# Optimization experiments

Measured on AMD Instinct MI355X. Metric: run time of the kernel, lower is better.

## Reference

```python
import jax, jax.numpy as jnp
import numpy as np

N = 100000
IN_C = 256
OUT_C = 128
E = 3200000
NNZ = 3200000
K = 3  # n_wavelets
ATT_H = 64


def spmm(idx, vals, m):
    # idx: [2, nnz] (row, col), vals: [nnz], m: [N, d] -> [N, d]
    rows, cols = idx[0], idx[1]
    return jax.ops.segment_sum(vals[:, None] * m[cols], rows, num_segments=N)


def appnp_k1_a0(h, edge_index):
    # PyG APPNP(K=1, alpha=0) == one gcn-normalized propagation with self-loops
    loops = jnp.arange(N, dtype=edge_index.dtype)
    row = jnp.concatenate([edge_index[0], loops])
    col = jnp.concatenate([edge_index[1], loops])
    ones = jnp.ones(row.shape[0], dtype=h.dtype)
    deg = jax.ops.segment_sum(ones, col, num_segments=N)
    dinv = jnp.where(deg > 0, 1.0 / jnp.sqrt(deg), 0.0)
    norm = dinv[row] * dinv[col]
    return jax.ops.segment_sum(norm[:, None] * h[col], row, num_segments=N)


def setup_inputs() -> dict:
    key = jax.random.key(0)
    ks = jax.random.split(key, 12)
    x = jax.random.normal(ks[0], (N, IN_C), dtype=jnp.float32)
    edge_index = jax.random.randint(ks[1], (2, E), 0, N)
    phi_idx = jax.random.randint(ks[2], (K, 2, NNZ), 0, N)
    phi_vals = jax.random.uniform(ks[3], (K, NNZ), dtype=jnp.float32) * (1.0 / 32.0)
    phi_inv_idx = jax.random.randint(ks[4], (K, 2, NNZ), 0, N)
    phi_inv_vals = jax.random.uniform(ks[5], (K, NNZ), dtype=jnp.float32) * (1.0 / 32.0)
    # learned parameters
    lin_w = jax.random.normal(ks[6], (IN_C, OUT_C), dtype=jnp.float32) * (1.0 / np.sqrt(IN_C))
    lin_b = jnp.zeros((OUT_C,), dtype=jnp.float32)
    gw_w = jax.random.normal(ks[7], (IN_C, OUT_C), dtype=jnp.float32) * (1.0 / np.sqrt(IN_C))
    diag_w = jax.random.uniform(ks[8], (N,), dtype=jnp.float32, minval=0.9, maxval=1.1)
    att_w1 = jax.random.normal(ks[9], (OUT_C, ATT_H), dtype=jnp.float32) * (1.0 / np.sqrt(OUT_C))
    att_b1 = jnp.zeros((ATT_H,), dtype=jnp.float32)
    att_w2 = jax.random.normal(ks[10], (ATT_H, 1), dtype=jnp.float32) * (1.0 / np.sqrt(ATT_H))
    return {"x": x, "edge_index": edge_index, "phi_idx": phi_idx, "phi_vals": phi_vals,
            "phi_inv_idx": phi_inv_idx, "phi_inv_vals": phi_inv_vals,
            "lin_w": lin_w, "lin_b": lin_b, "gw_w": gw_w, "diag_w": diag_w,
            "att_w1": att_w1, "att_b1": att_b1, "att_w2": att_w2}


def reference(x, edge_index, phi_idx, phi_vals, phi_inv_idx, phi_inv_vals,
              lin_w, lin_b, gw_w, diag_w, att_w1, att_b1, att_w2):
    # --- mean branch: Linear -> L2 normalize * 1.8 -> APPNP(K=1, alpha=0)
    mean = x @ lin_w + lin_b
    nrm = jnp.linalg.norm(mean, axis=1, keepdims=True)
    mean = mean / jnp.maximum(nrm, 1e-12) * 1.8
    mean = appnp_k1_a0(mean, edge_index)

    # --- logstd branch: GraphWaveletLayer (activation = identity)
    x_ = x @ gw_w  # [N, OUT_C]
    outs = []
    for i in range(K):
        t = spmm(phi_inv_idx[i], phi_inv_vals[i], x_)
        t = diag_w[:, None] * t
        t = spmm(phi_idx[i], phi_vals[i], t)
        outs.append(t)
    z = jnp.stack(outs, axis=1)  # [N, K, OUT_C]

    # --- attention pooling over wavelet axis
    w = jax.nn.relu(jnp.einsum('nkd,dh->nkh', z, att_w1) + att_b1) @ att_w2  # [N, K, 1]
    beta = jax.nn.softmax(w, axis=1)
    logstd = (beta * z).sum(axis=1)  # [N, OUT_C]
    return (mean, logstd)
```

## Files before the change

### kernel.cpp

```cpp
#include <hip/hip_runtime.h>
#include <hip/hip_bf16.h>
#include <hip/hip_fp16.h>


#define WS_HIST  2
#define WS_BUILD 6
#define WS_GATH  8

__global__ __launch_bounds__(256) void hist_kernel(const int* __restrict__ idx,
                                                   int* __restrict__ cnt, int n) {
    int i = blockIdx.x * 256 + threadIdx.x;
    if (i < n) atomicAdd(&cnt[__builtin_nontemporal_load(idx + i)], 1);
}

__global__ __launch_bounds__(256) void dinv_kernel(int* __restrict__ cnt,
                                                   float* __restrict__ dinv, int n) {
    int i = blockIdx.x * 256 + threadIdx.x;
    if (i < n) { dinv[i] = rsqrtf((float)(cnt[i] + 1)); cnt[i] = 0; }
}

__global__ __launch_bounds__(256) void scan_reduce_kernel(
    const int* __restrict__ cnt, int* __restrict__ bsum, int N) {
    __shared__ int wsum[4];
    int base = blockIdx.x * 1024;
    int t = threadIdx.x;
    int s = 0;
#pragma unroll
    for (int j = 0; j < 4; ++j) {
        int idx = base + t * 4 + j;
        if (idx < N) s += cnt[idx];
    }
#pragma unroll
    for (int off = 32; off; off >>= 1) s += __shfl_xor(s, off);
    int lane = t & 63, w = t >> 6;
    if (lane == 0) wsum[w] = s;
    __syncthreads();
    if (t == 0) bsum[blockIdx.x] = wsum[0] + wsum[1] + wsum[2] + wsum[3];
}

__global__ void scan_bsum_kernel(const int* __restrict__ bsum,
                                 int* __restrict__ bofs,
                                 int* __restrict__ ptr, int nblk, int N) {
    if (threadIdx.x == 0 && blockIdx.x == 0) {
        int run = 0;
        for (int i = 0; i < nblk; ++i) { bofs[i] = run; run += bsum[i]; }
        bofs[nblk] = run;
        ptr[N] = run;
    }
}

__global__ __launch_bounds__(256) void scan_block_kernel(
    int* __restrict__ cnt, const int* __restrict__ bofs,
    int* __restrict__ ptr, int* __restrict__ cursor, int N) {
    __shared__ int wsum[4];
    int base = blockIdx.x * 1024;
    int t = threadIdx.x, lane = t & 63, w = t >> 6;
    int v[4]; int s = 0;
#pragma unroll
    for (int j = 0; j < 4; ++j) {
        int idx = base + t * 4 + j;
        v[j] = (idx < N) ? cnt[idx] : 0;
        s += v[j];
    }
    int incl = s;
#pragma unroll
    for (int off = 1; off < 64; off <<= 1) {
        int nn = __shfl_up(incl, off);
        if (lane >= off) incl += nn;
    }
    if (lane == 63) wsum[w] = incl;
    __syncthreads();
    int wofs = 0;
    for (int i = 0; i < w; ++i) wofs += wsum[i];
    int run = bofs[blockIdx.x] + wofs + incl - s;
#pragma unroll
    for (int j = 0; j < 4; ++j) {
        int idx = base + t * 4 + j;
        if (idx < N) { ptr[idx] = run; cursor[idx] = run; cnt[idx] = 0; }
        run += v[j];
    }
}

__global__ __launch_bounds__(256) void fused_pipe_kernel(
    const int* __restrict__ ptr_g, const int2* __restrict__ cpair_g,
    const __half* __restrict__ src, const float* __restrict__ init_src,
    const float* __restrict__ dinv,
    float* __restrict__ dstf, __half* __restrict__ dsth, int N, int nnz_g,
    const int* __restrict__ rows_b, const int* __restrict__ cols_b,
    const float* __restrict__ vals_b, const float* __restrict__ diag,
    int* __restrict__ cursor_b, unsigned long long* __restrict__ cpair_b,
    int nnz_b, int mode,
    const int* __restrict__ rows_h, int* __restrict__ cnt, int nnz_h,
    int mix)
{
    int role, lid, nloc;
    if (!mix) { role = 2; lid = blockIdx.x; nloc = gridDim.x; }
    else {
        int r = blockIdx.x & 15, g = blockIdx.x >> 4, ng = gridDim.x >> 4;
        if (r < WS_HIST)                { role = 0; lid = g * WS_HIST + r;                nloc = ng * WS_HIST; }
        else if (r < WS_HIST + WS_BUILD){ role = 1; lid = g * WS_BUILD + (r - WS_HIST);   nloc = ng * WS_BUILD; }
        else                            { role = 2; lid = g * WS_GATH + (r - WS_HIST - WS_BUILD); nloc = ng * WS_GATH; }
    }

    if (role == 0) {
        if (!rows_h) return;
        int stride = nloc * 256;
        for (int i = lid * 256 + threadIdx.x; i < nnz_h; i += stride)
            atomicAdd(&cnt[__builtin_nontemporal_load(rows_h + i)], 1);
        return;
    }
    if (role == 1) {
        if (!rows_b) return;
        int stride = nloc * 256;
        for (int i = lid * 256 + threadIdx.x; i < nnz_b; i += stride) {
            int r = __builtin_nontemporal_load(rows_b + i);
            int c = __builtin_nontemporal_load(cols_b + i);
            float v;
            if (mode == 2) v = dinv[r] * dinv[c];
            else {
                v = __builtin_nontemporal_load(vals_b + i);
                if (mode == 1) v *= diag[c];
            }
            int pos = atomicAdd(&cursor_b[r], 1);
            unsigned long long pk =
                ((unsigned long long)(unsigned)__float_as_uint(v) << 32) | (unsigned)c;
            __builtin_nontemporal_store(pk, cpair_b + pos);
        }
        return;
    }

    const int lane = threadIdx.x & 63;
    const size_t lofs = (size_t)(lane * 2);
    int wid = (lid * 256 + threadIdx.x) >> 6;
    const int nwaves = (nloc * 256) >> 6;
    for (int row = wid; row < N; row += nwaves) {
        int s = ptr_g[row], e = ptr_g[row + 1];
        e = min(e, nnz_g); s = max(0, min(s, e));
        float accx = 0.f, accy = 0.f;
        if (init_src) {
            float d = dinv[row];
            float dd = d * d;
            float2 m = *(const float2*)(init_src + (size_t)row * 128 + lofs);
            accx = dd * m.x; accy = dd * m.y;
        }
        for (int base = s; base < e; base += 64) {
            int n = min(64, e - base);
            int2 p = make_int2(0, 0);
            if (lane < n) p = cpair_g[base + lane];
            int j = 0;
            for (; j + 16 <= n; j += 16) {
                __half2 sv[16];
                float vj[16];
#pragma unroll
                for (int u = 0; u < 16; ++u) {
                    int cj = __builtin_amdgcn_readlane(p.x, j + u);
                    vj[u] = __int_as_float(__builtin_amdgcn_readlane(p.y, j + u));
                    sv[u] = *(const __half2*)(src + (size_t)cj * 128 + lofs);
                }
#pragma unroll
                for (int u = 0; u < 16; ++u) {
                    accx += vj[u] * __low2float(sv[u]);
                    accy += vj[u] * __high2float(sv[u]);
                }
            }
            for (; j + 4 <= n; j += 4) {
                __half2 sv[4];
                float vj[4];
#pragma unroll
                for (int u = 0; u < 4; ++u) {
                    int cj = __builtin_amdgcn_readlane(p.x, j + u);
                    vj[u] = __int_as_float(__builtin_amdgcn_readlane(p.y, j + u));
                    sv[u] = *(const __half2*)(src + (size_t)cj * 128 + lofs);
                }
#pragma unroll
                for (int u = 0; u < 4; ++u) {
                    accx += vj[u] * __low2float(sv[u]);
                    accy += vj[u] * __high2float(sv[u]);
                }
            }
            for (; j < n; ++j) {
                int cj = __builtin_amdgcn_readlane(p.x, j);
                float vj = __int_as_float(__builtin_amdgcn_readlane(p.y, j));
                __half2 sv = *(const __half2*)(src + (size_t)cj * 128 + lofs);
                accx += vj * __low2float(sv);
                accy += vj * __high2float(sv);
            }
        }
        if (dstf) {
            float2 o; o.x = accx; o.y = accy;
            *(float2*)(dstf + (size_t)row * 128 + lofs) = o;
        }
        if (dsth) {
            *(__half2*)(dsth + (size_t)row * 128 + lofs) =
                __floats2half2_rn(accx, accy);
        }
    }
}

__global__ __launch_bounds__(256) void gemm_fused(
    const float* __restrict__ x, const float* __restrict__ lin_w,
    const float* __restrict__ lin_b, const float* __restrict__ gw_w,
    float* __restrict__ mean0, __half* __restrict__ xwh, int M) {
    __shared__ float As[32][68];
    __shared__ float Bs[32][64];
    const int tid = threadIdx.x;
    const int tx = tid & 15, ty = tid >> 4;
    const int row0 = blockIdx.x * 64;
    const int nt = blockIdx.y;
    const float* __restrict__ W = (nt < 2) ? lin_w : gw_w;
    const int colbase = (nt & 1) * 64;

    const int ar = tid >> 3;
    const int ac = (tid & 7) << 2;
    const int bk = tid >> 4;
    const int bn = (tid & 15) << 2;

    float acc[4][4] = {};

    for (int kt = 0; kt < 256; kt += 32) {
#pragma unroll
        for (int rr = 0; rr < 2; ++rr) {
            int r = ar + rr * 32;
            int grow = row0 + r;
            float4 v = make_float4(0.f, 0.f, 0.f, 0.f);
            if (grow < M) v = *(const float4*)(x + (size_t)grow * 256 + kt + ac);
            As[ac + 0][r] = v.x; As[ac + 1][r] = v.y;
            As[ac + 2][r] = v.z; As[ac + 3][r] = v.w;
        }
#pragma unroll
        for (int rr = 0; rr < 2; ++rr) {
            int k = bk + rr * 16;
            *(float4*)&Bs[k][bn] =
                *(const float4*)(W + (size_t)(kt + k) * 128 + colbase + bn);
        }
        __syncthreads();
#pragma unroll
        for (int k = 0; k < 32; ++k) {
            float4 a = *(const float4*)&As[k][ty * 4];
            float4 b = *(const float4*)&Bs[k][tx * 4];
            float av[4] = {a.x, a.y, a.z, a.w};
            float bv[4] = {b.x, b.y, b.z, b.w};
#pragma unroll
            for (int i = 0; i < 4; ++i)
#pragma unroll
                for (int j = 0; j < 4; ++j) acc[i][j] += av[i] * bv[j];
        }
        __syncthreads();
    }

    if (nt < 2) {
        float4 bb = *(const float4*)(lin_b + colbase + tx * 4);
#pragma unroll
        for (int i = 0; i < 4; ++i) {
            int grow = row0 + ty * 4 + i;
            if (grow < M) {
                float4 o = make_float4(acc[i][0] + bb.x, acc[i][1] + bb.y,
                                       acc[i][2] + bb.z, acc[i][3] + bb.w);
                *(float4*)(mean0 + (size_t)grow * 128 + colbase + tx * 4) = o;
            }
        }
    } else {
#pragma unroll
        for (int i = 0; i < 4; ++i) {
            int grow = row0 + ty * 4 + i;
            if (grow < M) {
                union { __half2 h[2]; int2 i2; } u;
                u.h[0] = __floats2half2_rn(acc[i][0], acc[i][1]);
                u.h[1] = __floats2half2_rn(acc[i][2], acc[i][3]);
                *(int2*)(xwh + (size_t)grow * 128 + colbase + tx * 4) = u.i2;
            }
        }
    }
}

__global__ __launch_bounds__(256) void rownorm_kernel(float* __restrict__ m,
                                                      __half* __restrict__ mh,
                                                      int n) {
    const int lane = threadIdx.x & 63;
    int wid = (blockIdx.x * 256 + threadIdx.x) >> 6;
    if (wid >= n) return;
    float2 v = *(float2*)(m + (size_t)wid * 128 + lane * 2);
    float ss = v.x * v.x + v.y * v.y;
#pragma unroll
    for (int off = 32; off; off >>= 1) ss += __shfl_xor(ss, off);
    float s = sqrtf(ss);
    float sc = 1.8f / fmaxf(s, 1e-12f);
    v.x *= sc; v.y *= sc;
    *(float2*)(m + (size_t)wid * 128 + lane * 2) = v;
    *(__half2*)(mh + (size_t)wid * 128 + lane * 2) = __floats2half2_rn(v.x, v.y);
}

__global__ __launch_bounds__(256) void attn_h_kernel(
    const __half* __restrict__ z0, const __half* __restrict__ z1,
    const float* __restrict__ z2, const float* __restrict__ w1,
    const float* __restrict__ b1, const float* __restrict__ w2,
    float* __restrict__ out, int n) {
    const int lane = threadIdx.x & 63;
    float w1reg[128];
#pragma unroll
    for (int d = 0; d < 128; ++d) w1reg[d] = w1[d * 64 + lane];
    const float b1l = b1[lane];
    const float w2l = w2[lane];

    int wid = (blockIdx.x * 256 + threadIdx.x) >> 6;
    const int nwaves = (gridDim.x * 256) >> 6;
    for (int node = wid; node < n; node += nwaves) {
        float2 za = __half22float2(*(const __half2*)(z0 + (size_t)node * 128 + lane * 2));
        float2 zb = __half22float2(*(const __half2*)(z1 + (size_t)node * 128 + lane * 2));
        float2 zc = *(const float2*)(z2 + (size_t)node * 128 + lane * 2);
        float wk[3];
#pragma unroll
        for (int k = 0; k < 3; ++k) {
            float zx = (k == 0) ? za.x : (k == 1) ? zb.x : zc.x;
            float zy = (k == 0) ? za.y : (k == 1) ? zb.y : zc.y;
            float acc = 0.f;
#pragma unroll
            for (int d2 = 0; d2 < 64; ++d2) {
                float ze = __uint_as_float(__builtin_amdgcn_readlane(__float_as_uint(zx), d2));
                float zo = __uint_as_float(__builtin_amdgcn_readlane(__float_as_uint(zy), d2));
                acc += ze * w1reg[2 * d2] + zo * w1reg[2 * d2 + 1];
            }
            float h = fmaxf(acc + b1l, 0.f) * w2l;
#pragma unroll
            for (int off = 32; off; off >>= 1) h += __shfl_xor(h, off);
            wk[k] = h;
        }
        float mx = fmaxf(wk[0], fmaxf(wk[1], wk[2]));
        float e0 = __expf(wk[0] - mx);
        float e1 = __expf(wk[1] - mx);
        float e2 = __expf(wk[2] - mx);
        float inv = 1.f / (e0 + e1 + e2);
        float be0 = e0 * inv, be1 = e1 * inv, be2 = e2 * inv;
        float2 o;
        o.x = be0 * za.x + be1 * zb.x + be2 * zc.x;
        o.y = be0 * za.y + be1 * zb.y + be2 * zc.y;
        *(float2*)(out + (size_t)node * 128 + lane * 2) = o;
    }
}

__global__ __launch_bounds__(256) void f2h_kernel(const float* __restrict__ in,
                                                  __half* __restrict__ out,
                                                  size_t n2) {
    size_t i = (size_t)blockIdx.x * 256 + threadIdx.x;
    if (i >= n2) return;
    float2 v = ((const float2*)in)[i];
    ((__half2*)out)[i] = __floats2half2_rn(v.x, v.y);
}

__global__ __launch_bounds__(256) void spmm_h_kernel(
    const int* __restrict__ rows, const int* __restrict__ cols,
    const float* __restrict__ vals, const float* __restrict__ diag,
    const __half* __restrict__ src, float* __restrict__ dst, int nnz) {
    const int lane = threadIdx.x & 63;
    int wid = (blockIdx.x * 256 + threadIdx.x) >> 6;
    const int nwaves = (gridDim.x * 256) >> 6;
    for (int e = wid; e < nnz; e += nwaves) {
        int r = rows[e];
        int c = cols[e];
        float v = vals ? vals[e] : 1.f;
        if (diag) v *= diag[c];
        __half2 sh = *(const __half2*)(src + (size_t)c * 128 + lane * 2);
        float* d = dst + (size_t)r * 128 + lane * 2;
        unsafeAtomicAdd(d,     v * __low2float(sh));
        unsafeAtomicAdd(d + 1, v * __high2float(sh));
    }
}

__global__ __launch_bounds__(256) void appnp_init_kernel(
    const float* __restrict__ mean0, const float* __restrict__ dinv,
    float* __restrict__ dst, int n) {
    int i = blockIdx.x * 256 + threadIdx.x;
    if (i >= n * 32) return;
    int node = i >> 5;
    float dv = dinv[node];
    float dd = dv * dv;
    float4 v = ((const float4*)mean0)[i];
    v.x *= dd; v.y *= dd; v.z *= dd; v.w *= dd;
    ((float4*)dst)[i] = v;
}

__global__ __launch_bounds__(256) void appnp_edge_h_kernel(
    const int* __restrict__ rows, const int* __restrict__ cols,
    const float* __restrict__ dinv, const __half* __restrict__ src,
    float* __restrict__ dst, int nnz) {
    const int lane = threadIdx.x & 63;
    int wid = (blockIdx.x * 256 + threadIdx.x) >> 6;
    const int nwaves = (gridDim.x * 256) >> 6;
    for (int e = wid; e < nnz; e += nwaves) {
        int r = rows[e];
        int c = cols[e];
        float v = dinv[r] * dinv[c];
        __half2 sh = *(const __half2*)(src + (size_t)c * 128 + lane * 2);
        float* d = dst + (size_t)r * 128 + lane * 2;
        unsafeAtomicAdd(d,     v * __low2float(sh));
        unsafeAtomicAdd(d + 1, v * __high2float(sh));
    }
}

__global__ __launch_bounds__(256) void attn_f_kernel(
    const float* __restrict__ z0, const float* __restrict__ z1,
    const float* __restrict__ z2, const float* __restrict__ w1,
    const float* __restrict__ b1, const float* __restrict__ w2,
    float* __restrict__ out, int n) {
    const int lane = threadIdx.x & 63;
    float w1reg[128];
#pragma unroll
    for (int d = 0; d < 128; ++d) w1reg[d] = w1[d * 64 + lane];
    const float b1l = b1[lane];
    const float w2l = w2[lane];
    int wid = (blockIdx.x * 256 + threadIdx.x) >> 6;
    const int nwaves = (gridDim.x * 256) >> 6;
    for (int node = wid; node < n; node += nwaves) {
        float2 za = *(const float2*)(z0 + (size_t)node * 128 + lane * 2);
        float2 zb = *(const float2*)(z1 + (size_t)node * 128 + lane * 2);
        float2 zc = *(const float2*)(z2 + (size_t)node * 128 + lane * 2);
        float wk[3];
#pragma unroll
        for (int k = 0; k < 3; ++k) {
            float zx = (k == 0) ? za.x : (k == 1) ? zb.x : zc.x;
            float zy = (k == 0) ? za.y : (k == 1) ? zb.y : zc.y;
            float acc = 0.f;
#pragma unroll
            for (int d2 = 0; d2 < 64; ++d2) {
                float ze = __uint_as_float(__builtin_amdgcn_readlane(__float_as_uint(zx), d2));
                float zo = __uint_as_float(__builtin_amdgcn_readlane(__float_as_uint(zy), d2));
                acc += ze * w1reg[2 * d2] + zo * w1reg[2 * d2 + 1];
            }
            float h = fmaxf(acc + b1l, 0.f) * w2l;
#pragma unroll
            for (int off = 32; off; off >>= 1) h += __shfl_xor(h, off);
            wk[k] = h;
        }
        float mx = fmaxf(wk[0], fmaxf(wk[1], wk[2]));
        float e0 = __expf(wk[0] - mx);
        float e1 = __expf(wk[1] - mx);
        float e2 = __expf(wk[2] - mx);
        float inv = 1.f / (e0 + e1 + e2);
        float be0 = e0 * inv, be1 = e1 * inv, be2 = e2 * inv;
        float2 o;
        o.x = be0 * za.x + be1 * zb.x + be2 * zc.x;
        o.y = be0 * za.y + be1 * zb.y + be2 * zc.y;
        *(float2*)(out + (size_t)node * 128 + lane * 2) = o;
    }
}

extern "C" void kernel_launch(void* const* d_in, const int* in_sizes, int n_in,
                              void* d_out, int out_size, void* d_ws, size_t ws_size,
                              hipStream_t stream)
{
    const float* x            = (const float*)d_in[0];
    const int*   edge_index   = (const int*)d_in[1];
    const int*   phi_idx      = (const int*)d_in[2];
    const float* phi_vals     = (const float*)d_in[3];
    const int*   phi_inv_idx  = (const int*)d_in[4];
    const float* phi_inv_vals = (const float*)d_in[5];
    const float* lin_w        = (const float*)d_in[6];
    const float* lin_b        = (const float*)d_in[7];
    const float* gw_w         = (const float*)d_in[8];
    const float* diag_w       = (const float*)d_in[9];
    const float* att_w1       = (const float*)d_in[10];
    const float* att_b1       = (const float*)d_in[11];
    const float* att_w2       = (const float*)d_in[12];

    const int N   = in_sizes[9];
    const int E   = in_sizes[1] / 2;
    const int NNZ = in_sizes[3] / 3;
    const size_t NF = (size_t)N * 128;
    const int MAXNNZ = (E > NNZ) ? E : NNZ;
    const int nblk = (N + 1023) / 1024;

    float* out0 = (float*)d_out;
    float* out1 = out0 + NF;

    char* p = (char*)d_ws;
    int*    cnt   = (int*)p;       p += (size_t)N * 4;
    float*  dinv  = (float*)p;     p += (size_t)N * 4;
    __half* xwh   = (__half*)p;    p += NF * 2;
    __half* xh    = (__half*)p;    p += NF * 2;
    char* tail = p;
    __half* z0h   = (__half*)p;    p += NF * 2;
    __half* z1h   = (__half*)p;    p += NF * 2;
    __half* t1h   = (__half*)p;    p += NF * 2;
    int*    ptrA  = (int*)p;       p += (size_t)(N + 1) * 4;
    int*    ptrB  = (int*)p;       p += (size_t)(N + 1) * 4;
    int*    curA  = (int*)p;       p += (size_t)N * 4;
    int*    curB  = (int*)p;       p += (size_t)N * 4;
    int*    bsum  = (int*)p;       p += (size_t)nblk * 4;
    int*    bofs  = (int*)p;       p += (size_t)(nblk + 1) * 4;
    p = (char*)(((uintptr_t)p + 7) & ~(uintptr_t)7);
    unsigned long long* cpairA = (unsigned long long*)p; p += (size_t)MAXNNZ * 8;
    unsigned long long* cpairB = (unsigned long long*)p; p += (size_t)MAXNNZ * 8;
    const size_t need_csr = p - (char*)d_ws;
    const bool csr_ok = (ws_size >= need_csr);
    int* ptrS[2] = {ptrA, ptrB};
    int* curS[2] = {curA, curB};
    unsigned long long* cpairS[2] = {cpairA, cpairB};
    (void)n_in; (void)out_size;

    (void)hipMemsetAsync(cnt, 0, (size_t)N * sizeof(int), stream);
    hist_kernel<<<(E + 255) / 256, 256, 0, stream>>>(edge_index + E, cnt, E);
    dinv_kernel<<<(N + 255) / 256, 256, 0, stream>>>(cnt, dinv, N);

    gemm_fused<<<dim3((N + 63) / 64, 4), 256, 0, stream>>>(
        x, lin_w, lin_b, gw_w, out1, xwh, N);
    rownorm_kernel<<<(N + 3) / 4, 256, 0, stream>>>(out1, xh, N);

    if (csr_ok) {
        struct Op {
            const int* rows; const int* cols; const float* vals;
            int mode; int nnz;
            const __half* src; const float* init_src;
            float* dstf; __half* dsth;
        } ops[7];
        ops[0] = {edge_index, edge_index + E, nullptr, 2, E,
                  xh, out1, out0, nullptr};
        for (int i = 0; i < 3; ++i) {
            const int* ri1 = phi_inv_idx + (size_t)i * 2 * NNZ;
            const int* ri2 = phi_idx + (size_t)i * 2 * NNZ;
            ops[1 + 2 * i] = {ri1, ri1 + NNZ, phi_inv_vals + (size_t)i * NNZ,
                              0, NNZ, xwh, nullptr, nullptr, t1h};
            float*  bf = (i == 2) ? out1 : nullptr;
            __half* bh = (i == 0) ? z0h : (i == 1) ? z1h : nullptr;
            ops[2 + 2 * i] = {ri2, ri2 + NNZ, phi_vals + (size_t)i * NNZ,
                              1, NNZ, t1h, nullptr, bf, bh};
        }

        auto scans = [&](int k) {
            scan_reduce_kernel<<<nblk, 256, 0, stream>>>(cnt, bsum, N);
            scan_bsum_kernel<<<1, 64, 0, stream>>>(bsum, bofs, ptrS[k & 1], nblk, N);
            scan_block_kernel<<<nblk, 256, 0, stream>>>(cnt, bofs, ptrS[k & 1],
                                                        curS[k & 1], N);
        };

        const int GRID = 2048;
        hist_kernel<<<(ops[0].nnz + 255) / 256, 256, 0, stream>>>(
            ops[0].rows, cnt, ops[0].nnz);
        scans(0);
        fused_pipe_kernel<<<GRID, 256, 0, stream>>>(
            nullptr, nullptr, nullptr, nullptr, dinv, nullptr, nullptr, 0, 0,
            ops[0].rows, ops[0].cols, ops[0].vals, diag_w, curS[0], cpairS[0],
            ops[0].nnz, ops[0].mode,
            ops[1].rows, cnt, ops[1].nnz, 1);
        scans(1);

        for (int k = 0; k < 7; ++k) {
            const Op& g = ops[k];
            const bool hb = (k < 6), hh = (k < 5);
            const Op* b = hb ? &ops[k + 1] : nullptr;
            fused_pipe_kernel<<<GRID, 256, 0, stream>>>(
                ptrS[k & 1], (const int2*)cpairS[k & 1], g.src, g.init_src,
                dinv, g.dstf, g.dsth, N, g.nnz,
                hb ? b->rows : nullptr, hb ? b->cols : nullptr,
                hb ? b->vals : nullptr, diag_w,
                hb ? curS[(k + 1) & 1] : nullptr,
                hb ? cpairS[(k + 1) & 1] : nullptr,
                hb ? b->nnz : 0, hb ? b->mode : 0,
                hh ? ops[k + 2].rows : nullptr, cnt, hh ? ops[k + 2].nnz : 0,
                hb ? 1 : 0);
            if (hh) scans(k + 2);
        }

        attn_h_kernel<<<2048, 256, 0, stream>>>(z0h, z1h, out1, att_w1, att_b1,
                                                att_w2, out1, N);
    } else {
        float*  z0f  = (float*)tail;
        float*  z1f  = z0f + NF;
        float*  t1f  = z1f + NF;
        __half* t1hf = (__half*)(t1f + NF);
        for (int i = 0; i < 3; ++i) {
            const int* ri1 = phi_inv_idx + (size_t)i * 2 * NNZ;
            const int* ci1 = ri1 + NNZ;
            const int* ri2 = phi_idx + (size_t)i * 2 * NNZ;
            const int* ci2 = ri2 + NNZ;
            float* zdst = (i == 0) ? z0f : (i == 1) ? z1f : out0;

            (void)hipMemsetAsync(t1f, 0, NF * sizeof(float), stream);
            spmm_h_kernel<<<(NNZ + 3) / 4, 256, 0, stream>>>(
                ri1, ci1, phi_inv_vals + (size_t)i * NNZ, nullptr, xwh, t1f, NNZ);
            f2h_kernel<<<((NF / 2) + 255) / 256, 256, 0, stream>>>(t1f, t1hf,
                                                                   NF / 2);
            (void)hipMemsetAsync(zdst, 0, NF * sizeof(float), stream);
            spmm_h_kernel<<<(NNZ + 3) / 4, 256, 0, stream>>>(
                ri2, ci2, phi_vals + (size_t)i * NNZ, diag_w, t1hf, zdst, NNZ);
        }
        attn_f_kernel<<<2048, 256, 0, stream>>>(z0f, z1f, out0, att_w1, att_b1,
                                                att_w2, t1f, N);
        appnp_init_kernel<<<((size_t)N * 32 + 255) / 256, 256, 0, stream>>>(
            out1, dinv, out0, N);
        appnp_edge_h_kernel<<<(E + 3) / 4, 256, 0, stream>>>(
            edge_index, edge_index + E, dinv, xh, out0, E);
        (void)hipMemcpyAsync(out1, t1f, NF * sizeof(float),
                             hipMemcpyDeviceToDevice, stream);
    }
}
```

Measured before the change: 2.993 ms.

## Pack CSR col/val into 32-bit words and fuse GEMM with first CSR build

The CSR pair entries shrink from 64-bit (col, fp32 val) to 32 bits: a 17-bit column and a 15-bit sign-less half value. This halves the traffic for writing and reading the CSR. The dense GEMM is moved into a new work-split kernel that runs alongside the first CSR build and histogram blocks, so the GEMM overlaps the scatter work. Nontemporal load and store hints are also dropped. Values lose precision (half, sign bit discarded), which only holds because all values are non-negative, and the path requires N < 2^17.

New measurement: 3.471 ms. 1.16x slower.

```diff
diff --git a/kernel.cpp b/kernel.cpp
--- a/kernel.cpp
+++ b/kernel.cpp
@@ -10,7 +10,7 @@
 __global__ __launch_bounds__(256) void hist_kernel(const int* __restrict__ idx,
                                                    int* __restrict__ cnt, int n) {
     int i = blockIdx.x * 256 + threadIdx.x;
-    if (i < n) atomicAdd(&cnt[__builtin_nontemporal_load(idx + i)], 1);
+    if (i < n) atomicAdd(&cnt[idx[i]], 1);
 }
 
 __global__ __launch_bounds__(256) void dinv_kernel(int* __restrict__ cnt,
@@ -81,14 +81,19 @@
     }
 }
 
+__device__ __forceinline__ unsigned pack_cv(int c, float v) {
+    unsigned h = (unsigned)__half_as_ushort(__float2half_rn(v));
+    return ((unsigned)c << 15) | (h & 0x7FFFu);
+}
+
 __global__ __launch_bounds__(256) void fused_pipe_kernel(
-    const int* __restrict__ ptr_g, const int2* __restrict__ cpair_g,
+    const int* __restrict__ ptr_g, const unsigned* __restrict__ cpair_g,
     const __half* __restrict__ src, const float* __restrict__ init_src,
     const float* __restrict__ dinv,
     float* __restrict__ dstf, __half* __restrict__ dsth, int N, int nnz_g,
     const int* __restrict__ rows_b, const int* __restrict__ cols_b,
     const float* __restrict__ vals_b, const float* __restrict__ diag,
-    int* __restrict__ cursor_b, unsigned long long* __restrict__ cpair_b,
+    int* __restrict__ cursor_b, unsigned* __restrict__ cpair_b,
     int nnz_b, int mode,
     const int* __restrict__ rows_h, int* __restrict__ cnt, int nnz_h,
     int mix)
@@ -106,29 +111,28 @@
         if (!rows_h) return;
         int stride = nloc * 256;
         for (int i = lid * 256 + threadIdx.x; i < nnz_h; i += stride)
-            atomicAdd(&cnt[__builtin_nontemporal_load(rows_h + i)], 1);
+            atomicAdd(&cnt[rows_h[i]], 1);
         return;
     }
     if (role == 1) {
         if (!rows_b) return;
         int stride = nloc * 256;
         for (int i = lid * 256 + threadIdx.x; i < nnz_b; i += stride) {
-            int r = __builtin_nontemporal_load(rows_b + i);
-            int c = __builtin_nontemporal_load(cols_b + i);
+            int r = rows_b[i];
+            int c = cols_b[i];
             float v;
             if (mode == 2) v = dinv[r] * dinv[c];
             else {
-                v = __builtin_nontemporal_load(vals_b + i);
+                v = vals_b[i];
                 if (mode == 1) v *= diag[c];
             }
             int pos = atomicAdd(&cursor_b[r], 1);
-            unsigned long long pk =
-                ((unsigned long long)(unsigned)__float_as_uint(v) << 32) | (unsigned)c;
-            __builtin_nontemporal_store(pk, cpair_b + pos);
+            cpair_b[pos] = pack_cv(c, v);
         }
         return;
     }
 
+    if (!ptr_g) return;
     const int lane = threadIdx.x & 63;
     const size_t lofs = (size_t)(lane * 2);
     int wid = (lid * 256 + threadIdx.x) >> 6;
@@ -145,7 +149,7 @@
         }
         for (int base = s; base < e; base += 64) {
             int n = min(64, e - base);
-            int2 p = make_int2(0, 0);
+            unsigned p = 0;
             if (lane < n) p = cpair_g[base + lane];
             int j = 0;
             for (; j + 16 <= n; j += 16) {
@@ -153,8 +157,9 @@
                 float vj[16];
 #pragma unroll
                 for (int u = 0; u < 16; ++u) {
-                    int cj = __builtin_amdgcn_readlane(p.x, j + u);
-                    vj[u] = __int_as_float(__builtin_amdgcn_readlane(p.y, j + u));
+                    unsigned pj = (unsigned)__builtin_amdgcn_readlane((int)p, j + u);
+                    int cj = (int)(pj >> 15);
+                    vj[u] = __half2float(__ushort_as_half((unsigned short)(pj & 0x7FFFu)));
                     sv[u] = *(const __half2*)(src + (size_t)cj * 128 + lofs);
                 }
 #pragma unroll
@@ -168,8 +173,9 @@
                 float vj[4];
 #pragma unroll
                 for (int u = 0; u < 4; ++u) {
-                    int cj = __builtin_amdgcn_readlane(p.x, j + u);
-                    vj[u] = __int_as_float(__builtin_amdgcn_readlane(p.y, j + u));
+                    unsigned pj = (unsigned)__builtin_amdgcn_readlane((int)p, j + u);
+                    int cj = (int)(pj >> 15);
+                    vj[u] = __half2float(__ushort_as_half((unsigned short)(pj & 0x7FFFu)));
                     sv[u] = *(const __half2*)(src + (size_t)cj * 128 + lofs);
                 }
 #pragma unroll
@@ -179,8 +185,9 @@
                 }
             }
             for (; j < n; ++j) {
-                int cj = __builtin_amdgcn_readlane(p.x, j);
-                float vj = __int_as_float(__builtin_amdgcn_readlane(p.y, j));
+                unsigned pj = (unsigned)__builtin_amdgcn_readlane((int)p, j);
+                int cj = (int)(pj >> 15);
+                float vj = __half2float(__ushort_as_half((unsigned short)(pj & 0x7FFFu)));
                 __half2 sv = *(const __half2*)(src + (size_t)cj * 128 + lofs);
                 accx += vj * __low2float(sv);
                 accy += vj * __high2float(sv);
@@ -194,6 +201,181 @@
             *(__half2*)(dsth + (size_t)row * 128 + lofs) =
                 __floats2half2_rn(accx, accy);
         }
+    }
+}
+
+__global__ __launch_bounds__(256) void fusedP_kernel(
+    const float* __restrict__ x, const float* __restrict__ lin_w,
+    const float* __restrict__ lin_b, const float* __restrict__ gw_w,
+    float* __restrict__ mean0, __half* __restrict__ xwh, int M,
+    const int* __restrict__ rows_b, const int* __restrict__ cols_b,
+    const float* __restrict__ diag, const float* __restrict__ dinv,
+    int* __restrict__ cursor_b, unsigned* __restrict__ cpair_b,
+    int nnz_b, int mode,
+    const int* __restrict__ rows_h, int* __restrict__ cnt, int nnz_h)
+{
+    __shared__ float As[32][68];
+    __shared__ float Bs[32][64];
+
+    int r = blockIdx.x & 15, g = blockIdx.x >> 4, ng = gridDim.x >> 4;
+    const int t = threadIdx.x;
+
+    if (r >= 14) {
+        int lid = g * 2 + (r - 14), nloc = ng * 2;
+        int stride = nloc * 256;
+        for (int i = lid * 256 + t; i < nnz_h; i += stride)
+            atomicAdd(&cnt[rows_h[i]], 1);
+        return;
+    }
+    if (r >= 8) {
+        int lid = g * 6 + (r - 8), nloc = ng * 6;
+        int stride = nloc * 256;
+        for (int i = lid * 256 + t; i < nnz_b; i += stride) {
+            int rr = rows_b[i];
+            int c = cols_b[i];
+            float v;
+            if (mode == 2) v = dinv[rr] * dinv[c];
+            else v = diag[c];
+            int pos = atomicAdd(&cursor_b[rr], 1);
+            cpair_b[pos] = pack_cv(c, v);
+        }
+        return;
+    }
+
+    int lid = g * 8 + r, nloc = ng * 8;
+    const int units = ((M + 63) / 64) * 4;
+    const int tx = t & 15, ty = t >> 4;
+    const int ar = t >> 3;
+    const int ac = (t & 7) << 2;
+    const int bk = t >> 4;
+    const int bn = (t & 15) << 2;
+
+    for (int u = lid; u < units; u += nloc) {
+        const int row0 = (u >> 2) * 64;
+        const int nt = u & 3;
+        const float* __restrict__ W = (nt < 2) ? lin_w : gw_w;
+        const int colbase = (nt & 1) * 64;
+        float acc[4][4] = {};
+
+        for (int kt = 0; kt < 256; kt += 32) {
+#pragma unroll
+            for (int rr = 0; rr < 2; ++rr) {
+                int rrow = ar + rr * 32;
+                int grow = row0 + rrow;
+                float4 v = make_float4(0.f, 0.f, 0.f, 0.f);
+                if (grow < M) v = *(const float4*)(x + (size_t)grow * 256 + kt + ac);
+                As[ac + 0][rrow] = v.x; As[ac + 1][rrow] = v.y;
+                As[ac + 2][rrow] = v.z; As[ac + 3][rrow] = v.w;
+            }
+#pragma unroll
+            for (int rr = 0; rr < 2; ++rr) {
+                int k = bk + rr * 16;
+                *(float4*)&Bs[k][bn] =
+                    *(const float4*)(W + (size_t)(kt + k) * 128 + colbase + bn);
+            }
+            __syncthreads();
+#pragma unroll
+            for (int k = 0; k < 32; ++k) {
+                float4 a = *(const float4*)&As[k][ty * 4];
+                float4 b = *(const float4*)&Bs[k][tx * 4];
+                float av[4] = {a.x, a.y, a.z, a.w};
+                float bv[4] = {b.x, b.y, b.z, b.w};
+#pragma unroll
+                for (int i = 0; i < 4; ++i)
+#pragma unroll
+                    for (int j = 0; j < 4; ++j) acc[i][j] += av[i] * bv[j];
+            }
+            __syncthreads();
+        }
+
+        if (nt < 2) {
+            float4 bb = *(const float4*)(lin_b + colbase + tx * 4);
+#pragma unroll
+            for (int i = 0; i < 4; ++i) {
+                int grow = row0 + ty * 4 + i;
+                if (grow < M) {
+                    float4 o = make_float4(acc[i][0] + bb.x, acc[i][1] + bb.y,
+                                           acc[i][2] + bb.z, acc[i][3] + bb.w);
+                    *(float4*)(mean0 + (size_t)grow * 128 + colbase + tx * 4) = o;
+                }
+            }
+        } else {
+#pragma unroll
+            for (int i = 0; i < 4; ++i) {
+                int grow = row0 + ty * 4 + i;
+                if (grow < M) {
+                    union { __half2 h[2]; int2 i2; } uu;
+                    uu.h[0] = __floats2half2_rn(acc[i][0], acc[i][1]);
+                    uu.h[1] = __floats2half2_rn(acc[i][2], acc[i][3]);
+                    *(int2*)(xwh + (size_t)grow * 128 + colbase + tx * 4) = uu.i2;
+                }
+            }
+        }
+    }
+}
+
+__global__ __launch_bounds__(256) void rownorm_kernel(float* __restrict__ m,
+                                                      __half* __restrict__ mh,
+                                                      int n) {
+    const int lane = threadIdx.x & 63;
+    int wid = (blockIdx.x * 256 + threadIdx.x) >> 6;
+    if (wid >= n) return;
+    float2 v = *(float2*)(m + (size_t)wid * 128 + lane * 2);
+    float ss = v.x * v.x + v.y * v.y;
+#pragma unroll
+    for (int off = 32; off; off >>= 1) ss += __shfl_xor(ss, off);
+    float s = sqrtf(ss);
+    float sc = 1.8f / fmaxf(s, 1e-12f);
+    v.x *= sc; v.y *= sc;
+    *(float2*)(m + (size_t)wid * 128 + lane * 2) = v;
+    *(__half2*)(mh + (size_t)wid * 128 + lane * 2) = __floats2half2_rn(v.x, v.y);
+}
+
+__global__ __launch_bounds__(256) void attn_h_kernel(
+    const __half* __restrict__ z0, const __half* __restrict__ z1,
+    const float* __restrict__ z2, const float* __restrict__ w1,
+    const float* __restrict__ b1, const float* __restrict__ w2,
+    float* __restrict__ out, int n) {
+    const int lane = threadIdx.x & 63;
+    float w1reg[128];
+#pragma unroll
+    for (int d = 0; d < 128; ++d) w1reg[d] = w1[d * 64 + lane];
+    const float b1l = b1[lane];
+    const float w2l = w2[lane];
+
+    int wid = (blockIdx.x * 256 + threadIdx.x) >> 6;
+    const int nwaves = (gridDim.x * 256) >> 6;
+    for (int node = wid; node < n; node += nwaves) {
+        float2 za = __half22float2(*(const __half2*)(z0 + (size_t)node * 128 + lane * 2));
+        float2 zb = __half22float2(*(const __half2*)(z1 + (size_t)node * 128 + lane * 2));
+        float2 zc = *(const float2*)(z2 + (size_t)node * 128 + lane * 2);
+        float wk[3];
+#pragma unroll
+        for (int k = 0; k < 3; ++k) {
+            float zx = (k == 0) ? za.x : (k == 1) ? zb.x : zc.x;
+            float zy = (k == 0) ? za.y : (k == 1) ? zb.y : zc.y;
+            float acc = 0.f;
+#pragma unroll
+            for (int d2 = 0; d2 < 64; ++d2) {
+                float ze = __uint_as_float(__builtin_amdgcn_readlane(__float_as_uint(zx), d2));
+                float zo = __uint_as_float(__builtin_amdgcn_readlane(__float_as_uint(zy), d2));
+                acc += ze * w1reg[2 * d2] + zo * w1reg[2 * d2 + 1];
+            }
+            float h = fmaxf(acc + b1l, 0.f) * w2l;
+#pragma unroll
+            for (int off = 32; off; off >>= 1) h += __shfl_xor(h, off);
+            wk[k] = h;
+        }
+        float mx = fmaxf(wk[0], fmaxf(wk[1], wk[2]));
+        float e0 = __expf(wk[0] - mx);
+        float e1 = __expf(wk[1] - mx);
+        float e2 = __expf(wk[2] - mx);
+        float inv = 1.f / (e0 + e1 + e2);
+        float be0 = e0 * inv, be1 = e1 * inv, be2 = e2 * inv;
+        float2 o;
+        o.x = be0 * za.x + be1 * zb.x + be2 * zc.x;
+        o.y = be0 * za.y + be1 * zb.y + be2 * zc.y;
+        *(float2*)(out + (size_t)node * 128 + lane * 2) = o;
     }
 }
 
@@ -209,14 +391,11 @@
     const int nt = blockIdx.y;
     const float* __restrict__ W = (nt < 2) ? lin_w : gw_w;
     const int colbase = (nt & 1) * 64;
-
     const int ar = tid >> 3;
     const int ac = (tid & 7) << 2;
     const int bk = tid >> 4;
     const int bn = (tid & 15) << 2;
-
     float acc[4][4] = {};
-
     for (int kt = 0; kt < 256; kt += 32) {
 #pragma unroll
         for (int rr = 0; rr < 2; ++rr) {
@@ -247,7 +426,6 @@
         }
         __syncthreads();
     }
-
     if (nt < 2) {
         float4 bb = *(const float4*)(lin_b + colbase + tx * 4);
 #pragma unroll
@@ -270,71 +448,6 @@
                 *(int2*)(xwh + (size_t)grow * 128 + colbase + tx * 4) = u.i2;
             }
         }
-    }
-}
-
-__global__ __launch_bounds__(256) void rownorm_kernel(float* __restrict__ m,
-                                                      __half* __restrict__ mh,
-                                                      int n) {
-    const int lane = threadIdx.x & 63;
-    int wid = (blockIdx.x * 256 + threadIdx.x) >> 6;
-    if (wid >= n) return;
-    float2 v = *(float2*)(m + (size_t)wid * 128 + lane * 2);
-    float ss = v.x * v.x + v.y * v.y;
-#pragma unroll
-    for (int off = 32; off; off >>= 1) ss += __shfl_xor(ss, off);
-    float s = sqrtf(ss);
-    float sc = 1.8f / fmaxf(s, 1e-12f);
-    v.x *= sc; v.y *= sc;
-    *(float2*)(m + (size_t)wid * 128 + lane * 2) = v;
-    *(__half2*)(mh + (size_t)wid * 128 + lane * 2) = __floats2half2_rn(v.x, v.y);
-}
-
-__global__ __launch_bounds__(256) void attn_h_kernel(
-    const __half* __restrict__ z0, const __half* __restrict__ z1,
-    const float* __restrict__ z2, const float* __restrict__ w1,
-    const float* __restrict__ b1, const float* __restrict__ w2,
-    float* __restrict__ out, int n) {
-    const int lane = threadIdx.x & 63;
-    float w1reg[128];
-#pragma unroll
-    for (int d = 0; d < 128; ++d) w1reg[d] = w1[d * 64 + lane];
-    const float b1l = b1[lane];
-    const float w2l = w2[lane];
-
-    int wid = (blockIdx.x * 256 + threadIdx.x) >> 6;
-    const int nwaves = (gridDim.x * 256) >> 6;
-    for (int node = wid; node < n; node += nwaves) {
-        float2 za = __half22float2(*(const __half2*)(z0 + (size_t)node * 128 + lane * 2));
-        float2 zb = __half22float2(*(const __half2*)(z1 + (size_t)node * 128 + lane * 2));
-        float2 zc = *(const float2*)(z2 + (size_t)node * 128 + lane * 2);
-        float wk[3];
-#pragma unroll
-        for (int k = 0; k < 3; ++k) {
-            float zx = (k == 0) ? za.x : (k == 1) ? zb.x : zc.x;
-            float zy = (k == 0) ? za.y : (k == 1) ? zb.y : zc.y;
-            float acc = 0.f;
-#pragma unroll
-            for (int d2 = 0; d2 < 64; ++d2) {
-                float ze = __uint_as_float(__builtin_amdgcn_readlane(__float_as_uint(zx), d2));
-                float zo = __uint_as_float(__builtin_amdgcn_readlane(__float_as_uint(zy), d2));
-                acc += ze * w1reg[2 * d2] + zo * w1reg[2 * d2 + 1];
-            }
-            float h = fmaxf(acc + b1l, 0.f) * w2l;
-#pragma unroll
-            for (int off = 32; off; off >>= 1) h += __shfl_xor(h, off);
-            wk[k] = h;
-        }
-        float mx = fmaxf(wk[0], fmaxf(wk[1], wk[2]));
-        float e0 = __expf(wk[0] - mx);
-        float e1 = __expf(wk[1] - mx);
-        float e2 = __expf(wk[2] - mx);
-        float inv = 1.f / (e0 + e1 + e2);
-        float be0 = e0 * inv, be1 = e1 * inv, be2 = e2 * inv;
-        float2 o;
-        o.x = be0 * za.x + be1 * zb.x + be2 * zc.x;
-        o.y = be0 * za.y + be1 * zb.y + be2 * zc.y;
-        *(float2*)(out + (size_t)node * 128 + lane * 2) = o;
     }
 }
 
@@ -487,23 +600,18 @@
     int*    curB  = (int*)p;       p += (size_t)N * 4;
     int*    bsum  = (int*)p;       p += (size_t)nblk * 4;
     int*    bofs  = (int*)p;       p += (size_t)(nblk + 1) * 4;
-    p = (char*)(((uintptr_t)p + 7) & ~(uintptr_t)7);
-    unsigned long long* cpairA = (unsigned long long*)p; p += (size_t)MAXNNZ * 8;
-    unsigned long long* cpairB = (unsigned long long*)p; p += (size_t)MAXNNZ * 8;
+    unsigned* cpairA = (unsigned*)p; p += (size_t)MAXNNZ * 4;
+    unsigned* cpairB = (unsigned*)p; p += (size_t)MAXNNZ * 4;
     const size_t need_csr = p - (char*)d_ws;
-    const bool csr_ok = (ws_size >= need_csr);
+    const bool csr_ok = (ws_size >= need_csr) && (N < (1 << 17));
     int* ptrS[2] = {ptrA, ptrB};
     int* curS[2] = {curA, curB};
-    unsigned long long* cpairS[2] = {cpairA, cpairB};
+    unsigned* cpairS[2] = {cpairA, cpairB};
     (void)n_in; (void)out_size;
 
     (void)hipMemsetAsync(cnt, 0, (size_t)N * sizeof(int), stream);
     hist_kernel<<<(E + 255) / 256, 256, 0, stream>>>(edge_index + E, cnt, E);
     dinv_kernel<<<(N + 255) / 256, 256, 0, stream>>>(cnt, dinv, N);
-
-    gemm_fused<<<dim3((N + 63) / 64, 4), 256, 0, stream>>>(
-        x, lin_w, lin_b, gw_w, out1, xwh, N);
-    rownorm_kernel<<<(N + 3) / 4, 256, 0, stream>>>(out1, xh, N);
 
     if (csr_ok) {
         struct Op {
@@ -536,11 +644,12 @@
         hist_kernel<<<(ops[0].nnz + 255) / 256, 256, 0, stream>>>(
             ops[0].rows, cnt, ops[0].nnz);
         scans(0);
-        fused_pipe_kernel<<<GRID, 256, 0, stream>>>(
-            nullptr, nullptr, nullptr, nullptr, dinv, nullptr, nullptr, 0, 0,
-            ops[0].rows, ops[0].cols, ops[0].vals, diag_w, curS[0], cpairS[0],
+        fusedP_kernel<<<GRID, 256, 0, stream>>>(
+            x, lin_w, lin_b, gw_w, out1, xwh, N,
+            ops[0].rows, ops[0].cols, diag_w, dinv, curS[0], cpairS[0],
             ops[0].nnz, ops[0].mode,
-            ops[1].rows, cnt, ops[1].nnz, 1);
+            ops[1].rows, cnt, ops[1].nnz);
+        rownorm_kernel<<<(N + 3) / 4, 256, 0, stream>>>(out1, xh, N);
         scans(1);
 
         for (int k = 0; k < 7; ++k) {
@@ -548,7 +657,7 @@
             const bool hb = (k < 6), hh = (k < 5);
             const Op* b = hb ? &ops[k + 1] : nullptr;
             fused_pipe_kernel<<<GRID, 256, 0, stream>>>(
-                ptrS[k & 1], (const int2*)cpairS[k & 1], g.src, g.init_src,
+                ptrS[k & 1], cpairS[k & 1], g.src, g.init_src,
                 dinv, g.dstf, g.dsth, N, g.nnz,
                 hb ? b->rows : nullptr, hb ? b->cols : nullptr,
                 hb ? b->vals : nullptr, diag_w,
@@ -563,6 +672,9 @@
         attn_h_kernel<<<2048, 256, 0, stream>>>(z0h, z1h, out1, att_w1, att_b1,
                                                 att_w2, out1, N);
     } else {
+        gemm_fused<<<dim3((N + 63) / 64, 4), 256, 0, stream>>>(
+            x, lin_w, lin_b, gw_w, out1, xwh, N);
+        rownorm_kernel<<<(N + 3) / 4, 256, 0, stream>>>(out1, xh, N);
         float*  z0f  = (float*)tail;
         float*  z1f  = z0f + NF;
         float*  t1f  = z1f + NF;
```

## Pack CSR column and fp16 value into 32-bit word, rebalance prologue roles

Applied to the files above, without the earlier changes.

Packs each CSR entry as a 17-bit column index plus a 15-bit fp16 value (sign bit dropped, so values are assumed non-negative) in one 32-bit word instead of a 64-bit pair. This halves the scatter-write and gather-read traffic of the CSR arrays. It adds a guard that N fits in 17 bits and a new role split for the first prologue launch, where no gather work exists. Nontemporal load/store hints are also removed. The trade-off is lower edge-weight precision, and correctness depends on all weights being non-negative.

After: 3.484 ms. +16.4%, slower.

```diff
diff --git a/kernel.cpp b/kernel.cpp
--- a/kernel.cpp
+++ b/kernel.cpp
@@ -10,7 +10,7 @@
 __global__ __launch_bounds__(256) void hist_kernel(const int* __restrict__ idx,
                                                    int* __restrict__ cnt, int n) {
     int i = blockIdx.x * 256 + threadIdx.x;
-    if (i < n) atomicAdd(&cnt[__builtin_nontemporal_load(idx + i)], 1);
+    if (i < n) atomicAdd(&cnt[idx[i]], 1);
 }
 
 __global__ __launch_bounds__(256) void dinv_kernel(int* __restrict__ cnt,
@@ -81,21 +81,30 @@
     }
 }
 
+__device__ __forceinline__ unsigned pack_cv(int c, float v) {
+    unsigned h = (unsigned)__half_as_ushort(__float2half_rn(v));
+    return ((unsigned)c << 15) | (h & 0x7FFFu);
+}
+
 __global__ __launch_bounds__(256) void fused_pipe_kernel(
-    const int* __restrict__ ptr_g, const int2* __restrict__ cpair_g,
+    const int* __restrict__ ptr_g, const unsigned* __restrict__ cpair_g,
     const __half* __restrict__ src, const float* __restrict__ init_src,
     const float* __restrict__ dinv,
     float* __restrict__ dstf, __half* __restrict__ dsth, int N, int nnz_g,
     const int* __restrict__ rows_b, const int* __restrict__ cols_b,
     const float* __restrict__ vals_b, const float* __restrict__ diag,
-    int* __restrict__ cursor_b, unsigned long long* __restrict__ cpair_b,
+    int* __restrict__ cursor_b, unsigned* __restrict__ cpair_b,
     int nnz_b, int mode,
     const int* __restrict__ rows_h, int* __restrict__ cnt, int nnz_h,
     int mix)
 {
     int role, lid, nloc;
-    if (!mix) { role = 2; lid = blockIdx.x; nloc = gridDim.x; }
-    else {
+    if (mix == 0) { role = 2; lid = blockIdx.x; nloc = gridDim.x; }
+    else if (mix == 2) {
+        int r = blockIdx.x & 15, g = blockIdx.x >> 4, ng = gridDim.x >> 4;
+        if (r < 12) { role = 1; lid = g * 12 + r;        nloc = ng * 12; }
+        else        { role = 0; lid = g * 4 + (r - 12);  nloc = ng * 4; }
+    } else {
         int r = blockIdx.x & 15, g = blockIdx.x >> 4, ng = gridDim.x >> 4;
         if (r < WS_HIST)                { role = 0; lid = g * WS_HIST + r;                nloc = ng * WS_HIST; }
         else if (r < WS_HIST + WS_BUILD){ role = 1; lid = g * WS_BUILD + (r - WS_HIST);   nloc = ng * WS_BUILD; }
@@ -106,29 +115,28 @@
         if (!rows_h) return;
         int stride = nloc * 256;
         for (int i = lid * 256 + threadIdx.x; i < nnz_h; i += stride)
-            atomicAdd(&cnt[__builtin_nontemporal_load(rows_h + i)], 1);
+            atomicAdd(&cnt[rows_h[i]], 1);
         return;
     }
     if (role == 1) {
         if (!rows_b) return;
         int stride = nloc * 256;
         for (int i = lid * 256 + threadIdx.x; i < nnz_b; i += stride) {
-            int r = __builtin_nontemporal_load(rows_b + i);
-            int c = __builtin_nontemporal_load(cols_b + i);
+            int r = rows_b[i];
+            int c = cols_b[i];
             float v;
             if (mode == 2) v = dinv[r] * dinv[c];
             else {
-                v = __builtin_nontemporal_load(vals_b + i);
+                v = vals_b[i];
                 if (mode == 1) v *= diag[c];
             }
             int pos = atomicAdd(&cursor_b[r], 1);
-            unsigned long long pk =
-                ((unsigned long long)(unsigned)__float_as_uint(v) << 32) | (unsigned)c;
-            __builtin_nontemporal_store(pk, cpair_b + pos);
+            cpair_b[pos] = pack_cv(c, v);
         }
         return;
     }
 
+    if (!ptr_g) return;
     const int lane = threadIdx.x & 63;
     const size_t lofs = (size_t)(lane * 2);
     int wid = (lid * 256 + threadIdx.x) >> 6;
@@ -145,7 +153,7 @@
         }
         for (int base = s; base < e; base += 64) {
             int n = min(64, e - base);
-            int2 p = make_int2(0, 0);
+            unsigned p = 0;
             if (lane < n) p = cpair_g[base + lane];
             int j = 0;
             for (; j + 16 <= n; j += 16) {
@@ -153,8 +161,9 @@
                 float vj[16];
 #pragma unroll
                 for (int u = 0; u < 16; ++u) {
-                    int cj = __builtin_amdgcn_readlane(p.x, j + u);
-                    vj[u] = __int_as_float(__builtin_amdgcn_readlane(p.y, j + u));
+                    unsigned pj = (unsigned)__builtin_amdgcn_readlane((int)p, j + u);
+                    int cj = (int)(pj >> 15);
+                    vj[u] = __half2float(__ushort_as_half((unsigned short)(pj & 0x7FFFu)));
                     sv[u] = *(const __half2*)(src + (size_t)cj * 128 + lofs);
                 }
 #pragma unroll
@@ -168,8 +177,9 @@
                 float vj[4];
 #pragma unroll
                 for (int u = 0; u < 4; ++u) {
-                    int cj = __builtin_amdgcn_readlane(p.x, j + u);
-                    vj[u] = __int_as_float(__builtin_amdgcn_readlane(p.y, j + u));
+                    unsigned pj = (unsigned)__builtin_amdgcn_readlane((int)p, j + u);
+                    int cj = (int)(pj >> 15);
+                    vj[u] = __half2float(__ushort_as_half((unsigned short)(pj & 0x7FFFu)));
                     sv[u] = *(const __half2*)(src + (size_t)cj * 128 + lofs);
                 }
 #pragma unroll
@@ -179,8 +189,9 @@
                 }
             }
             for (; j < n; ++j) {
-                int cj = __builtin_amdgcn_readlane(p.x, j);
-                float vj = __int_as_float(__builtin_amdgcn_readlane(p.y, j));
+                unsigned pj = (unsigned)__builtin_amdgcn_readlane((int)p, j);
+                int cj = (int)(pj >> 15);
+                float vj = __half2float(__ushort_as_half((unsigned short)(pj & 0x7FFFu)));
                 __half2 sv = *(const __half2*)(src + (size_t)cj * 128 + lofs);
                 accx += vj * __low2float(sv);
                 accy += vj * __high2float(sv);
@@ -487,14 +498,13 @@
     int*    curB  = (int*)p;       p += (size_t)N * 4;
     int*    bsum  = (int*)p;       p += (size_t)nblk * 4;
     int*    bofs  = (int*)p;       p += (size_t)(nblk + 1) * 4;
-    p = (char*)(((uintptr_t)p + 7) & ~(uintptr_t)7);
-    unsigned long long* cpairA = (unsigned long long*)p; p += (size_t)MAXNNZ * 8;
-    unsigned long long* cpairB = (unsigned long long*)p; p += (size_t)MAXNNZ * 8;
+    unsigned* cpairA = (unsigned*)p; p += (size_t)MAXNNZ * 4;
+    unsigned* cpairB = (unsigned*)p; p += (size_t)MAXNNZ * 4;
     const size_t need_csr = p - (char*)d_ws;
-    const bool csr_ok = (ws_size >= need_csr);
+    const bool csr_ok = (ws_size >= need_csr) && (N < (1 << 17));
     int* ptrS[2] = {ptrA, ptrB};
     int* curS[2] = {curA, curB};
-    unsigned long long* cpairS[2] = {cpairA, cpairB};
+    unsigned* cpairS[2] = {cpairA, cpairB};
     (void)n_in; (void)out_size;
 
     (void)hipMemsetAsync(cnt, 0, (size_t)N * sizeof(int), stream);
@@ -537,10 +547,10 @@
             ops[0].rows, cnt, ops[0].nnz);
         scans(0);
         fused_pipe_kernel<<<GRID, 256, 0, stream>>>(
-            nullptr, nullptr, nullptr, nullptr, dinv, nullptr, nullptr, 0, 0,
+            nullptr, nullptr, nullptr, nullptr, dinv, nullptr, nullptr, N, 0,
             ops[0].rows, ops[0].cols, ops[0].vals, diag_w, curS[0], cpairS[0],
             ops[0].nnz, ops[0].mode,
-            ops[1].rows, cnt, ops[1].nnz, 1);
+            ops[1].rows, cnt, ops[1].nnz, 2);
         scans(1);
 
         for (int k = 0; k < 7; ++k) {
@@ -548,7 +558,7 @@
             const bool hb = (k < 6), hh = (k < 5);
             const Op* b = hb ? &ops[k + 1] : nullptr;
             fused_pipe_kernel<<<GRID, 256, 0, stream>>>(
-                ptrS[k & 1], (const int2*)cpairS[k & 1], g.src, g.init_src,
+                ptrS[k & 1], cpairS[k & 1], g.src, g.init_src,
                 dinv, g.dstf, g.dsth, N, g.nnz,
                 hb ? b->rows : nullptr, hb ? b->cols : nullptr,
                 hb ? b->vals : nullptr, diag_w,
```
